# Kernel optimization log

Hardware: AMD Instinct MI355X
Metric: run time of the kernel (lower is better)

## Reference

```python
import jax, jax.numpy as jnp
import numpy as np

N_NODES = 50000


def gcn_conv(x, edge_index, W, b):
    # PyG GCNConv: add self-loops, symmetric normalization, then aggregate.
    n = x.shape[0]
    loop = jnp.arange(n, dtype=edge_index.dtype)
    src = jnp.concatenate([edge_index[0], loop])  # [E+N]
    dst = jnp.concatenate([edge_index[1], loop])  # [E+N]
    deg = jax.ops.segment_sum(jnp.ones_like(dst, dtype=x.dtype), dst, num_segments=n)
    dinv = jnp.where(deg > 0, jax.lax.rsqrt(deg), 0.0)
    norm = dinv[src] * dinv[dst]                  # [E+N]
    xw = x @ W                                     # [N, out]
    msg = xw[src] * norm[:, None]                  # [E+N, out]
    out = jax.ops.segment_sum(msg, dst, num_segments=n)
    return out + b


def setup_inputs() -> dict:
    key = jax.random.key(0)
    ks = jax.random.split(key, 8)
    n, e, d, h, c = N_NODES, 800000, 128, 128, 40
    x = jax.random.normal(ks[0], (n, d), dtype=jnp.float32)
    edge_index = jax.random.randint(ks[1], (2, e), 0, n, dtype=jnp.int64)
    s = 0.05
    W1 = jax.random.normal(ks[2], (d, h), dtype=jnp.float32) * s
    b1 = jnp.zeros((h,), dtype=jnp.float32)
    W2 = jax.random.normal(ks[3], (h, h), dtype=jnp.float32) * s
    b2 = jnp.zeros((h,), dtype=jnp.float32)
    W3 = jax.random.normal(ks[4], (h, c), dtype=jnp.float32) * s
    b3 = jnp.zeros((c,), dtype=jnp.float32)
    return {"x": x, "edge_index": edge_index, "W1": W1, "b1": b1,
            "W2": W2, "b2": b2, "W3": W3, "b3": b3}


def reference(x, edge_index, W1, b1, W2, b2, W3, b3):
    # Block 0: GCNConv -> relu -> (dropout: identity in eval) -> residual
    h = jax.nn.relu(gcn_conv(x, edge_index, W1, b1)) + x
    # Block 1: GCNConv -> relu -> (dropout: identity in eval) -> residual
    h = jax.nn.relu(gcn_conv(h, edge_index, W2, b2)) + h
    # Final conv + log_softmax over classes
    out = gcn_conv(h, edge_index, W3, b3)
    return jax.nn.log_softmax(out, axis=1)
```

## Files before the change

kernel.cpp:

```cpp
#include <hip/hip_runtime.h>
#include <math.h>


#define HD 128
#define NC 40

typedef __attribute__((ext_vector_type(8))) short bfrag;
typedef __attribute__((ext_vector_type(4))) float facc;

__device__ __forceinline__ float4 fma4(float s, float4 w, float4 a) {
  a.x = fmaf(s, w.x, a.x);
  a.y = fmaf(s, w.y, a.y);
  a.z = fmaf(s, w.z, a.z);
  a.w = fmaf(s, w.w, a.w);
  return a;
}

__device__ __forceinline__ unsigned short f2bf(float f) {
  unsigned int u = __float_as_uint(f);
  u += 0x7FFFu + ((u >> 16) & 1u);
  return (unsigned short)(u >> 16);
}
__device__ __forceinline__ unsigned int packbf2(float a, float b) {
  return (unsigned int)f2bf(a) | ((unsigned int)f2bf(b) << 16);
}
__device__ __forceinline__ float bf2f(unsigned short v) {
  return __uint_as_float((unsigned int)v << 16);
}
__device__ __forceinline__ float2 bf2f2(unsigned int v) {
  float2 r;
  r.x = __uint_as_float(v << 16);
  r.y = __uint_as_float(v & 0xFFFF0000u);
  return r;
}
__device__ __forceinline__ float db(unsigned int u, int i) {
  return (float)(signed char)((u >> (8 * i)) & 0xFFu);
}

#define NCOPY 8


__global__ void k_init(int* __restrict__ cnt8, int* __restrict__ gtotal, int n8) {
  int i = blockIdx.x * 256 + threadIdx.x;
  if (i < n8) cnt8[i] = 0;
  if (i == 0) *gtotal = 0;
}

__global__ __launch_bounds__(256) void k_count_rank(
    const int* __restrict__ dst, int* __restrict__ cnt8,
    int* __restrict__ rank, int E, int n) {
  int e = blockIdx.x * 256 + threadIdx.x;
  if (e < E) {
    int copy = blockIdx.x & (NCOPY - 1);
    rank[e] = atomicAdd(&cnt8[copy * n + dst[e]], 1);
  }
}

__global__ __launch_bounds__(256) void k_alloc(
    const int* __restrict__ cnt8, int* __restrict__ row_start,
    int* __restrict__ row_end, int2* __restrict__ cinfo,
    float* __restrict__ dinv, int* __restrict__ gtotal, int n) {
  __shared__ int sh[256];
  __shared__ int base_sh;
  const int tid = threadIdx.x;
  int i = blockIdx.x * 256 + tid;
  int c[NCOPY];
  int v = 0;
  if (i < n) {
#pragma unroll
    for (int j = 0; j < NCOPY; ++j) {
      c[j] = cnt8[j * n + i];
      v += c[j];
    }
  }
  sh[tid] = v;
  __syncthreads();
  for (int off = 1; off < 256; off <<= 1) {
    int t = (tid >= off) ? sh[tid - off] : 0;
    __syncthreads();
    sh[tid] += t;
    __syncthreads();
  }
  if (tid == 255) base_sh = atomicAdd(gtotal, sh[255]);
  __syncthreads();
  if (i < n) {
    int start = base_sh + sh[tid] - v;
    float dv = rsqrtf((float)(v + 1));
    row_start[i] = start;
    row_end[i] = start + v;
    dinv[i] = dv;
    int base = start;
#pragma unroll
    for (int j = 0; j < NCOPY; ++j) {
      cinfo[(size_t)j * n + i] = make_int2(base, __float_as_int(dv));
      base += c[j];
    }
  }
}

__global__ __launch_bounds__(256) void k_fill(
    const int* __restrict__ src, const int* __restrict__ dst,
    const int* __restrict__ rank, const int2* __restrict__ cinfo,
    const float* __restrict__ dinv, int2* __restrict__ csr2, int E, int n) {
  int t = blockIdx.x * 256 + threadIdx.x;
  int nt = gridDim.x * 256;
#pragma unroll
  for (int q = 0; q < 4; ++q) {
    int e = t + q * nt;
    if (e < E) {
      int d = dst[e];
      int s = src[e];
      int r = rank[e];
      int copy = (e >> 8) & (NCOPY - 1);
      int2 ni = cinfo[(size_t)copy * n + d];
      float norm = dinv[s] * __int_as_float(ni.y);
      csr2[ni.x + r] = make_int2(s, __float_as_int(norm));
    }
  }
}


__global__ __launch_bounds__(256) void k_wprep(
    const float* __restrict__ W1, const float* __restrict__ W2,
    unsigned short* __restrict__ W1t, unsigned short* __restrict__ W2t) {
  const float* W = blockIdx.x ? W2 : W1;
  unsigned short* Wt = blockIdx.x ? W2t : W1t;
  __shared__ unsigned short sh[HD * 136];
#pragma unroll
  for (int i = 0; i < 16; ++i) {
    int f4 = i * 256 + threadIdx.x;
    int r = f4 >> 5;
    int c = (f4 & 31) * 4;
    float4 v = *(const float4*)(W + r * HD + c);
    sh[(c + 0) * 136 + r] = f2bf(v.x);
    sh[(c + 1) * 136 + r] = f2bf(v.y);
    sh[(c + 2) * 136 + r] = f2bf(v.z);
    sh[(c + 3) * 136 + r] = f2bf(v.w);
  }
  __syncthreads();
#pragma unroll
  for (int i = 0; i < 8; ++i) {
    int g = i * 256 + threadIdx.x;
    int nrow = g >> 4, k16 = g & 15;
    uint4 v = *(const uint4*)(&sh[nrow * 136 + k16 * 8]);
    *(uint4*)(Wt + (size_t)g * 8) = v;
  }
}


template <bool A_IS_F32>
__global__ __launch_bounds__(256) void gemm_mfma_f128(
    const float* __restrict__ Af, const unsigned short* __restrict__ Ab,
    const unsigned short* __restrict__ Wt,
    signed char* __restrict__ xw8, float* __restrict__ xscale, int n) {
  __shared__ unsigned short shWt[HD * 136];
  {
#pragma unroll
    for (int i = 0; i < 8; ++i) {
      int g = i * 256 + threadIdx.x;
      int nrow = g >> 4, k16 = g & 15;
      uint4 v = *(const uint4*)(Wt + (size_t)g * 8);
      *(uint4*)(&shWt[nrow * 136 + k16 * 8]) = v;
    }
  }

  const int lane = threadIdx.x & 63;
  const int w = threadIdx.x >> 6;
  const int m = blockIdx.x * 64 + w * 16 + (lane & 15);
  const int mc = min(m, n - 1);
  const int kbase = (lane >> 4) * 8;

  bfrag af[4];
  if constexpr (A_IS_F32) {
    const float* ap = Af + (size_t)mc * HD + kbase;
#pragma unroll
    for (int kk = 0; kk < 4; ++kk) {
      float4 lo = *(const float4*)(ap + kk * 32);
      float4 hi = *(const float4*)(ap + kk * 32 + 4);
      bfrag a;
      a[0] = (short)f2bf(lo.x); a[1] = (short)f2bf(lo.y);
      a[2] = (short)f2bf(lo.z); a[3] = (short)f2bf(lo.w);
      a[4] = (short)f2bf(hi.x); a[5] = (short)f2bf(hi.y);
      a[6] = (short)f2bf(hi.z); a[7] = (short)f2bf(hi.w);
      af[kk] = a;
    }
  } else {
    const unsigned short* ap = Ab + (size_t)mc * HD + kbase;
#pragma unroll
    for (int kk = 0; kk < 4; ++kk) af[kk] = *(const bfrag*)(ap + kk * 32);
  }

  __syncthreads();

  facc acc[8];
#pragma unroll
  for (int c = 0; c < 8; ++c) {
    acc[c][0] = 0.f; acc[c][1] = 0.f; acc[c][2] = 0.f; acc[c][3] = 0.f;
  }

#pragma unroll
  for (int kk = 0; kk < 4; ++kk) {
#pragma unroll
    for (int c = 0; c < 8; ++c) {
      bfrag bf = *(const bfrag*)(&shWt[(c * 16 + (lane & 15)) * 136 + kk * 32 + kbase]);
      acc[c] = __builtin_amdgcn_mfma_f32_16x16x32_bf16(af[kk], bf, acc[c], 0, 0, 0);
    }
  }

  float rmax[4];
#pragma unroll
  for (int q = 0; q < 4; ++q) {
    float mx = 0.f;
#pragma unroll
    for (int c = 0; c < 8; ++c) mx = fmaxf(mx, fabsf(acc[c][q]));
    rmax[q] = mx;
  }
#pragma unroll
  for (int off = 1; off < 16; off <<= 1) {
#pragma unroll
    for (int q = 0; q < 4; ++q) rmax[q] = fmaxf(rmax[q], __shfl_xor(rmax[q], off, 64));
  }

  const int rbase = blockIdx.x * 64 + w * 16 + (lane >> 4) * 4;
  const int col = lane & 15;
#pragma unroll
  for (int q = 0; q < 4; ++q) {
    int r = rbase + q;
    if (r < n) {
      float inv = (rmax[q] > 0.f) ? (127.f / rmax[q]) : 0.f;
      if (col == q) xscale[r] = rmax[q] * (1.f / 127.f);
#pragma unroll
      for (int c = 0; c < 8; ++c) {
        int v = __float2int_rn(acc[c][q] * inv);
        xw8[(size_t)r * HD + c * 16 + col] = (signed char)v;
      }
    }
  }
}


__global__ __launch_bounds__(320) void gemm_k128_f40(
    const float* __restrict__ A, const float* __restrict__ W,
    unsigned short* __restrict__ out, int n) {
  __shared__ float shW[HD * NC];
  {
    const float4* Wv = (const float4*)W;
    float4* shWv = (float4*)shW;
    for (int t = threadIdx.x; t < HD * NC / 4; t += 320) shWv[t] = Wv[t];
  }
  __syncthreads();

  const int cg = threadIdx.x % 10;
  const int rg = threadIdx.x / 10;
  const int jg = cg * 4;
  const int row0 = blockIdx.x * 128 + rg * 4;
  const int nm1 = n - 1;
  const float* a[4];
#pragma unroll
  for (int r = 0; r < 4; ++r) a[r] = A + (size_t)min(row0 + r, nm1) * HD;

  float4 acc[4];
#pragma unroll
  for (int r = 0; r < 4; ++r) acc[r] = make_float4(0.f, 0.f, 0.f, 0.f);

  for (int k = 0; k < HD; k += 4) {
    const float* wb = shW + k * NC + jg;
    float4 w0 = *(const float4*)(wb);
    float4 w1 = *(const float4*)(wb + NC);
    float4 w2 = *(const float4*)(wb + 2 * NC);
    float4 w3 = *(const float4*)(wb + 3 * NC);
#pragma unroll
    for (int r = 0; r < 4; ++r) {
      float4 xv = *(const float4*)(a[r] + k);
      acc[r] = fma4(xv.w, w3, fma4(xv.z, w2, fma4(xv.y, w1, fma4(xv.x, w0, acc[r]))));
    }
  }
#pragma unroll
  for (int r = 0; r < 4; ++r) {
    if (row0 + r < n) {
      uint2 p;
      p.x = packbf2(acc[r].x, acc[r].y);
      p.y = packbf2(acc[r].z, acc[r].w);
      *(uint2*)(out + (size_t)(row0 + r) * NC + jg) = p;
    }
  }
}


__global__ __launch_bounds__(256) void agg_f128(
    const signed char* __restrict__ xw8, const float* __restrict__ xscale,
    const float* __restrict__ resid, const float* __restrict__ bias,
    const float* __restrict__ dinv,
    const int* __restrict__ row_start, const int* __restrict__ row_end,
    const int2* __restrict__ csr2, float* __restrict__ out,
    unsigned short* __restrict__ hb, int n) {
  const int node = (blockIdx.x * 256 + threadIdx.x) >> 4;
  if (node >= n) return;
  const int li = threadIdx.x & 15;
  const int f0 = li * 8;

  float di = dinv[node];
  float4 b01 = *(const float4*)(bias + f0);
  float4 b23 = *(const float4*)(bias + f0 + 4);
  uint2 su = *(const uint2*)(xw8 + (size_t)node * HD + f0);
  float ssc = xscale[node] * di * di;
  float a0 = fmaf(db(su.x, 0), ssc, b01.x);
  float a1 = fmaf(db(su.x, 1), ssc, b01.y);
  float a2 = fmaf(db(su.x, 2), ssc, b01.z);
  float a3 = fmaf(db(su.x, 3), ssc, b01.w);
  float a4 = fmaf(db(su.y, 0), ssc, b23.x);
  float a5 = fmaf(db(su.y, 1), ssc, b23.y);
  float a6 = fmaf(db(su.y, 2), ssc, b23.z);
  float a7 = fmaf(db(su.y, 3), ssc, b23.w);

  int k = row_start[node];
  const int end = row_end[node];
  for (; k + 4 <= end; k += 4) {
    int2 c0 = csr2[k], c1 = csr2[k + 1], c2 = csr2[k + 2], c3 = csr2[k + 3];
    uint2 u0 = *(const uint2*)(xw8 + (size_t)c0.x * HD + f0);
    uint2 u1 = *(const uint2*)(xw8 + (size_t)c1.x * HD + f0);
    uint2 u2 = *(const uint2*)(xw8 + (size_t)c2.x * HD + f0);
    uint2 u3 = *(const uint2*)(xw8 + (size_t)c3.x * HD + f0);
    float w0 = __int_as_float(c0.y) * xscale[c0.x];
    float w1 = __int_as_float(c1.y) * xscale[c1.x];
    float w2 = __int_as_float(c2.y) * xscale[c2.x];
    float w3 = __int_as_float(c3.y) * xscale[c3.x];
    a0 = fmaf(db(u0.x, 0), w0, a0); a1 = fmaf(db(u0.x, 1), w0, a1);
    a2 = fmaf(db(u0.x, 2), w0, a2); a3 = fmaf(db(u0.x, 3), w0, a3);
    a4 = fmaf(db(u0.y, 0), w0, a4); a5 = fmaf(db(u0.y, 1), w0, a5);
    a6 = fmaf(db(u0.y, 2), w0, a6); a7 = fmaf(db(u0.y, 3), w0, a7);
    a0 = fmaf(db(u1.x, 0), w1, a0); a1 = fmaf(db(u1.x, 1), w1, a1);
    a2 = fmaf(db(u1.x, 2), w1, a2); a3 = fmaf(db(u1.x, 3), w1, a3);
    a4 = fmaf(db(u1.y, 0), w1, a4); a5 = fmaf(db(u1.y, 1), w1, a5);
    a6 = fmaf(db(u1.y, 2), w1, a6); a7 = fmaf(db(u1.y, 3), w1, a7);
    a0 = fmaf(db(u2.x, 0), w2, a0); a1 = fmaf(db(u2.x, 1), w2, a1);
    a2 = fmaf(db(u2.x, 2), w2, a2); a3 = fmaf(db(u2.x, 3), w2, a3);
    a4 = fmaf(db(u2.y, 0), w2, a4); a5 = fmaf(db(u2.y, 1), w2, a5);
    a6 = fmaf(db(u2.y, 2), w2, a6); a7 = fmaf(db(u2.y, 3), w2, a7);
    a0 = fmaf(db(u3.x, 0), w3, a0); a1 = fmaf(db(u3.x, 1), w3, a1);
    a2 = fmaf(db(u3.x, 2), w3, a2); a3 = fmaf(db(u3.x, 3), w3, a3);
    a4 = fmaf(db(u3.y, 0), w3, a4); a5 = fmaf(db(u3.y, 1), w3, a5);
    a6 = fmaf(db(u3.y, 2), w3, a6); a7 = fmaf(db(u3.y, 3), w3, a7);
  }
  for (; k < end; ++k) {
    int2 c = csr2[k];
    uint2 u = *(const uint2*)(xw8 + (size_t)c.x * HD + f0);
    float w = __int_as_float(c.y) * xscale[c.x];
    a0 = fmaf(db(u.x, 0), w, a0); a1 = fmaf(db(u.x, 1), w, a1);
    a2 = fmaf(db(u.x, 2), w, a2); a3 = fmaf(db(u.x, 3), w, a3);
    a4 = fmaf(db(u.y, 0), w, a4); a5 = fmaf(db(u.y, 1), w, a5);
    a6 = fmaf(db(u.y, 2), w, a6); a7 = fmaf(db(u.y, 3), w, a7);
  }

  float4 r0 = *(const float4*)(resid + (size_t)node * HD + f0);
  float4 r1 = *(const float4*)(resid + (size_t)node * HD + f0 + 4);
  float4 o0, o1;
  o0.x = fmaxf(a0, 0.f) + r0.x; o0.y = fmaxf(a1, 0.f) + r0.y;
  o0.z = fmaxf(a2, 0.f) + r0.z; o0.w = fmaxf(a3, 0.f) + r0.w;
  o1.x = fmaxf(a4, 0.f) + r1.x; o1.y = fmaxf(a5, 0.f) + r1.y;
  o1.z = fmaxf(a6, 0.f) + r1.z; o1.w = fmaxf(a7, 0.f) + r1.w;
  *(float4*)(out + (size_t)node * HD + f0) = o0;
  *(float4*)(out + (size_t)node * HD + f0 + 4) = o1;
  if (hb) {
    uint4 hv;
    hv.x = packbf2(o0.x, o0.y);
    hv.y = packbf2(o0.z, o0.w);
    hv.z = packbf2(o1.x, o1.y);
    hv.w = packbf2(o1.z, o1.w);
    *(uint4*)(hb + (size_t)node * HD + f0) = hv;
  }
}


__global__ __launch_bounds__(256) void agg_f40_lsm(
    const unsigned short* __restrict__ xw, const float* __restrict__ dinv,
    const int* __restrict__ row_start, const int* __restrict__ row_end,
    const int2* __restrict__ csr2, const float* __restrict__ bias,
    float* __restrict__ out, int n) {
  const int node = (blockIdx.x * 256 + threadIdx.x) >> 4;
  if (node >= n) return;
  const int li = threadIdx.x & 15;
  const bool act = li < 10;
  const int f0 = li * 4;

  float a0 = 0.f, a1 = 0.f, a2 = 0.f, a3 = 0.f;
  float di = dinv[node];
  if (act) {
    float4 bv = *(const float4*)(bias + f0);
    uint2 su = *(const uint2*)(xw + (size_t)node * NC + f0);
    float2 s0 = bf2f2(su.x), s1 = bf2f2(su.y);
    float ssc = di * di;
    a0 = fmaf(s0.x, ssc, bv.x);
    a1 = fmaf(s0.y, ssc, bv.y);
    a2 = fmaf(s1.x, ssc, bv.z);
    a3 = fmaf(s1.y, ssc, bv.w);
  }

  int k = row_start[node];
  const int end = row_end[node];
  for (; k + 4 <= end; k += 4) {
    int2 c0 = csr2[k], c1 = csr2[k + 1], c2 = csr2[k + 2], c3 = csr2[k + 3];
    if (act) {
      uint2 u0 = *(const uint2*)(xw + (size_t)c0.x * NC + f0);
      uint2 u1 = *(const uint2*)(xw + (size_t)c1.x * NC + f0);
      uint2 u2 = *(const uint2*)(xw + (size_t)c2.x * NC + f0);
      uint2 u3 = *(const uint2*)(xw + (size_t)c3.x * NC + f0);
      float w0 = __int_as_float(c0.y), w1 = __int_as_float(c1.y);
      float w2 = __int_as_float(c2.y), w3 = __int_as_float(c3.y);
      float2 p, q;
      p = bf2f2(u0.x); q = bf2f2(u0.y);
      a0 = fmaf(p.x, w0, a0); a1 = fmaf(p.y, w0, a1);
      a2 = fmaf(q.x, w0, a2); a3 = fmaf(q.y, w0, a3);
      p = bf2f2(u1.x); q = bf2f2(u1.y);
      a0 = fmaf(p.x, w1, a0); a1 = fmaf(p.y, w1, a1);
      a2 = fmaf(q.x, w1, a2); a3 = fmaf(q.y, w1, a3);
      p = bf2f2(u2.x); q = bf2f2(u2.y);
      a0 = fmaf(p.x, w2, a0); a1 = fmaf(p.y, w2, a1);
      a2 = fmaf(q.x, w2, a2); a3 = fmaf(q.y, w2, a3);
      p = bf2f2(u3.x); q = bf2f2(u3.y);
      a0 = fmaf(p.x, w3, a0); a1 = fmaf(p.y, w3, a1);
      a2 = fmaf(q.x, w3, a2); a3 = fmaf(q.y, w3, a3);
    }
  }
  for (; k < end; ++k) {
    int2 c = csr2[k];
    if (act) {
      uint2 u = *(const uint2*)(xw + (size_t)c.x * NC + f0);
      float w = __int_as_float(c.y);
      float2 p = bf2f2(u.x), q = bf2f2(u.y);
      a0 = fmaf(p.x, w, a0); a1 = fmaf(p.y, w, a1);
      a2 = fmaf(q.x, w, a2); a3 = fmaf(q.y, w, a3);
    }
  }

  float m = act ? fmaxf(fmaxf(a0, a1), fmaxf(a2, a3)) : -3.0e38f;
  m = fmaxf(m, __shfl_xor(m, 1, 64));
  m = fmaxf(m, __shfl_xor(m, 2, 64));
  m = fmaxf(m, __shfl_xor(m, 4, 64));
  m = fmaxf(m, __shfl_xor(m, 8, 64));
  float s = act ? (expf(a0 - m) + expf(a1 - m) + expf(a2 - m) + expf(a3 - m)) : 0.f;
  s += __shfl_xor(s, 1, 64);
  s += __shfl_xor(s, 2, 64);
  s += __shfl_xor(s, 4, 64);
  s += __shfl_xor(s, 8, 64);
  if (act) {
    float lse = m + logf(s);
    float4 o;
    o.x = a0 - lse; o.y = a1 - lse; o.z = a2 - lse; o.w = a3 - lse;
    *(float4*)(out + (size_t)node * NC + f0) = o;
  }
}


extern "C" void kernel_launch(void* const* d_in, const int* in_sizes, int n_in,
                              void* d_out, int out_size, void* d_ws, size_t ws_size,
                              hipStream_t stream) {
  const float* x  = (const float*)d_in[0];
  const int*   ei = (const int*)d_in[1];
  const float* W1 = (const float*)d_in[2];
  const float* b1 = (const float*)d_in[3];
  const float* W2 = (const float*)d_in[4];
  const float* b2 = (const float*)d_in[5];
  const float* W3 = (const float*)d_in[6];
  const float* b3 = (const float*)d_in[7];
  float* out = (float*)d_out;

  const int n = in_sizes[0] / HD;
  const int E = in_sizes[1] / 2;
  const int* src = ei;
  const int* dst = ei + E;

  char* ws = (char*)d_ws;
  size_t off = 0;
  auto carve = [&](size_t bytes) -> void* {
    void* p = ws + off;
    off += (bytes + 255) & ~(size_t)255;
    return p;
  };
  int*   cnt8      = (int*)carve((size_t)n * NCOPY * 4);
  int*   row_start = (int*)carve((size_t)n * 4);
  int*   row_end   = (int*)carve((size_t)n * 4);
  float* dinv      = (float*)carve((size_t)n * 4);
  int2*  cinfo     = (int2*)carve((size_t)n * NCOPY * 8);
  int*   gtotal    = (int*)carve(256);
  unsigned short* w1t = (unsigned short*)carve((size_t)HD * HD * 2);
  unsigned short* w2t = (unsigned short*)carve((size_t)HD * HD * 2);
  int2*  csr2      = (int2*)carve((size_t)E * 8);
  signed char* xw8 = (signed char*)carve((size_t)n * HD);
  float* xscale    = (float*)carve((size_t)n * 4);
  unsigned short* xw40 = (unsigned short*)carve((size_t)n * NC * 2);
  unsigned short* hb  = (unsigned short*)carve((size_t)n * HD * 2);
  float* bufB      = (float*)carve((size_t)n * HD * 4);
  int*   rank      = (int*)bufB;

  const int gn8  = (n * NCOPY + 255) / 256;
  const int gE1  = (E + 255) / 256;
  const int gE4  = (E + 1023) / 1024;
  const int gA   = (n + 15) / 16;
  const int gM   = (n + 63) / 64;
  const int g40  = (n + 127) / 128;

  k_init<<<gn8, 256, 0, stream>>>(cnt8, gtotal, n * NCOPY);
  k_wprep<<<2, 256, 0, stream>>>(W1, W2, w1t, w2t);
  k_count_rank<<<gE1, 256, 0, stream>>>(dst, cnt8, rank, E, n);
  k_alloc<<<(n + 255) / 256, 256, 0, stream>>>(cnt8, row_start, row_end, cinfo, dinv, gtotal, n);
  k_fill<<<gE4, 256, 0, stream>>>(src, dst, rank, cinfo, dinv, csr2, E, n);

  gemm_mfma_f128<true><<<gM, 256, 0, stream>>>(x, (const unsigned short*)nullptr, w1t, xw8, xscale, n);
  agg_f128<<<gA, 256, 0, stream>>>(xw8, xscale, x, b1, dinv, row_start, row_end, csr2, bufB, hb, n);

  gemm_mfma_f128<false><<<gM, 256, 0, stream>>>((const float*)nullptr, hb, w2t, xw8, xscale, n);
  agg_f128<<<gA, 256, 0, stream>>>(xw8, xscale, bufB, b2, dinv, row_start, row_end, csr2, bufB,
                                   (unsigned short*)nullptr, n);

  gemm_k128_f40<<<g40, 320, 0, stream>>>(bufB, W3, xw40, n);
  agg_f40_lsm<<<gA, 256, 0, stream>>>(xw40, dinv, row_start, row_end, csr2, b3, out, n);
}
```

Measured before the change: 186.4 us.

## Use bf16 MFMA for final 40-class GEMM and skip fp32 layer-2 output

Result: faster. 168.2 us (-9.7%).

```diff
diff --git a/kernel.cpp b/kernel.cpp
--- a/kernel.cpp
+++ b/kernel.cpp
@@ -7,14 +7,6 @@
 
 typedef __attribute__((ext_vector_type(8))) short bfrag;
 typedef __attribute__((ext_vector_type(4))) float facc;
-
-__device__ __forceinline__ float4 fma4(float s, float4 w, float4 a) {
-  a.x = fmaf(s, w.x, a.x);
-  a.y = fmaf(s, w.y, a.y);
-  a.z = fmaf(s, w.z, a.z);
-  a.w = fmaf(s, w.w, a.w);
-  return a;
-}
 
 __device__ __forceinline__ unsigned short f2bf(float f) {
   unsigned int u = __float_as_uint(f);
@@ -23,9 +15,6 @@
 }
 __device__ __forceinline__ unsigned int packbf2(float a, float b) {
   return (unsigned int)f2bf(a) | ((unsigned int)f2bf(b) << 16);
-}
-__device__ __forceinline__ float bf2f(unsigned short v) {
-  return __uint_as_float((unsigned int)v << 16);
 }
 __device__ __forceinline__ float2 bf2f2(unsigned int v) {
   float2 r;
@@ -102,20 +91,15 @@
     const int* __restrict__ src, const int* __restrict__ dst,
     const int* __restrict__ rank, const int2* __restrict__ cinfo,
     const float* __restrict__ dinv, int2* __restrict__ csr2, int E, int n) {
-  int t = blockIdx.x * 256 + threadIdx.x;
-  int nt = gridDim.x * 256;
-#pragma unroll
-  for (int q = 0; q < 4; ++q) {
-    int e = t + q * nt;
-    if (e < E) {
-      int d = dst[e];
-      int s = src[e];
-      int r = rank[e];
-      int copy = (e >> 8) & (NCOPY - 1);
-      int2 ni = cinfo[(size_t)copy * n + d];
-      float norm = dinv[s] * __int_as_float(ni.y);
-      csr2[ni.x + r] = make_int2(s, __float_as_int(norm));
-    }
+  int e = blockIdx.x * 256 + threadIdx.x;
+  if (e < E) {
+    int d = dst[e];
+    int s = src[e];
+    int r = rank[e];
+    int copy = (e >> 8) & (NCOPY - 1);
+    int2 ni = cinfo[(size_t)copy * n + d];
+    float norm = dinv[s] * __int_as_float(ni.y);
+    csr2[ni.x + r] = make_int2(s, __float_as_int(norm));
   }
 }
 
@@ -147,6 +131,34 @@
   }
 }
 
+__global__ __launch_bounds__(256) void k_wprep3(
+    const float* __restrict__ W3, unsigned short* __restrict__ W3t) {
+  __shared__ unsigned short sh[48 * 136];
+  for (int i = threadIdx.x; i < 48 * 136; i += 256) sh[i] = 0;
+  __syncthreads();
+#pragma unroll
+  for (int i = 0; i < 5; ++i) {
+    int f4 = i * 256 + threadIdx.x;
+    if (f4 < 1280) {
+      int r = f4 / 10;
+      int c = (f4 % 10) * 4;
+      float4 v = *(const float4*)(W3 + r * NC + c);
+      sh[(c + 0) * 136 + r] = f2bf(v.x);
+      sh[(c + 1) * 136 + r] = f2bf(v.y);
+      sh[(c + 2) * 136 + r] = f2bf(v.z);
+      sh[(c + 3) * 136 + r] = f2bf(v.w);
+    }
+  }
+  __syncthreads();
+#pragma unroll
+  for (int i = 0; i < 3; ++i) {
+    int g = i * 256 + threadIdx.x;
+    int nrow = g >> 4, k16 = g & 15;
+    uint4 v = *(const uint4*)(&sh[nrow * 136 + k16 * 8]);
+    *(uint4*)(W3t + (size_t)g * 8) = v;
+  }
+}
+
 
 template <bool A_IS_F32>
 __global__ __launch_bounds__(256) void gemm_mfma_f128(
@@ -239,49 +251,59 @@
 }
 
 
-__global__ __launch_bounds__(320) void gemm_k128_f40(
-    const float* __restrict__ A, const float* __restrict__ W,
+__global__ __launch_bounds__(256) void gemm_mfma_f40(
+    const unsigned short* __restrict__ Ab,
+    const unsigned short* __restrict__ Wt,
     unsigned short* __restrict__ out, int n) {
-  __shared__ float shW[HD * NC];
+  __shared__ unsigned short shWt[48 * 136];
   {
-    const float4* Wv = (const float4*)W;
-    float4* shWv = (float4*)shW;
-    for (int t = threadIdx.x; t < HD * NC / 4; t += 320) shWv[t] = Wv[t];
-  }
-  __syncthreads();
-
-  const int cg = threadIdx.x % 10;
-  const int rg = threadIdx.x / 10;
-  const int jg = cg * 4;
-  const int row0 = blockIdx.x * 128 + rg * 4;
-  const int nm1 = n - 1;
-  const float* a[4];
-#pragma unroll
-  for (int r = 0; r < 4; ++r) a[r] = A + (size_t)min(row0 + r, nm1) * HD;
-
-  float4 acc[4];
-#pragma unroll
-  for (int r = 0; r < 4; ++r) acc[r] = make_float4(0.f, 0.f, 0.f, 0.f);
-
-  for (int k = 0; k < HD; k += 4) {
-    const float* wb = shW + k * NC + jg;
-    float4 w0 = *(const float4*)(wb);
-    float4 w1 = *(const float4*)(wb + NC);
-    float4 w2 = *(const float4*)(wb + 2 * NC);
-    float4 w3 = *(const float4*)(wb + 3 * NC);
-#pragma unroll
-    for (int r = 0; r < 4; ++r) {
-      float4 xv = *(const float4*)(a[r] + k);
-      acc[r] = fma4(xv.w, w3, fma4(xv.z, w2, fma4(xv.y, w1, fma4(xv.x, w0, acc[r]))));
-    }
-  }
-#pragma unroll
-  for (int r = 0; r < 4; ++r) {
-    if (row0 + r < n) {
-      uint2 p;
-      p.x = packbf2(acc[r].x, acc[r].y);
-      p.y = packbf2(acc[r].z, acc[r].w);
-      *(uint2*)(out + (size_t)(row0 + r) * NC + jg) = p;
+#pragma unroll
+    for (int i = 0; i < 3; ++i) {
+      int g = i * 256 + threadIdx.x;
+      int nrow = g >> 4, k16 = g & 15;
+      uint4 v = *(const uint4*)(Wt + (size_t)g * 8);
+      *(uint4*)(&shWt[nrow * 136 + k16 * 8]) = v;
+    }
+  }
+
+  const int lane = threadIdx.x & 63;
+  const int w = threadIdx.x >> 6;
+  const int m = blockIdx.x * 64 + w * 16 + (lane & 15);
+  const int mc = min(m, n - 1);
+  const int kbase = (lane >> 4) * 8;
+
+  bfrag af[4];
+  const unsigned short* ap = Ab + (size_t)mc * HD + kbase;
+#pragma unroll
+  for (int kk = 0; kk < 4; ++kk) af[kk] = *(const bfrag*)(ap + kk * 32);
+
+  __syncthreads();
+
+  facc acc[3];
+#pragma unroll
+  for (int c = 0; c < 3; ++c) {
+    acc[c][0] = 0.f; acc[c][1] = 0.f; acc[c][2] = 0.f; acc[c][3] = 0.f;
+  }
+#pragma unroll
+  for (int kk = 0; kk < 4; ++kk) {
+#pragma unroll
+    for (int c = 0; c < 3; ++c) {
+      bfrag bf = *(const bfrag*)(&shWt[(c * 16 + (lane & 15)) * 136 + kk * 32 + kbase]);
+      acc[c] = __builtin_amdgcn_mfma_f32_16x16x32_bf16(af[kk], bf, acc[c], 0, 0, 0);
+    }
+  }
+
+  const int rbase = blockIdx.x * 64 + w * 16 + (lane >> 4) * 4;
+  const int col = lane & 15;
+#pragma unroll
+  for (int c = 0; c < 3; ++c) {
+    int j = c * 16 + col;
+    if (j < NC) {
+#pragma unroll
+      for (int q = 0; q < 4; ++q) {
+        int r = rbase + q;
+        if (r < n) out[(size_t)r * NC + j] = f2bf(acc[c][q]);
+      }
     }
   }
 }
@@ -359,8 +381,10 @@
   o0.z = fmaxf(a2, 0.f) + r0.z; o0.w = fmaxf(a3, 0.f) + r0.w;
   o1.x = fmaxf(a4, 0.f) + r1.x; o1.y = fmaxf(a5, 0.f) + r1.y;
   o1.z = fmaxf(a6, 0.f) + r1.z; o1.w = fmaxf(a7, 0.f) + r1.w;
-  *(float4*)(out + (size_t)node * HD + f0) = o0;
-  *(float4*)(out + (size_t)node * HD + f0 + 4) = o1;
+  if (out) {
+    *(float4*)(out + (size_t)node * HD + f0) = o0;
+    *(float4*)(out + (size_t)node * HD + f0 + 4) = o1;
+  }
   if (hb) {
     uint4 hv;
     hv.x = packbf2(o0.x, o0.y);
@@ -485,6 +509,7 @@
   int*   gtotal    = (int*)carve(256);
   unsigned short* w1t = (unsigned short*)carve((size_t)HD * HD * 2);
   unsigned short* w2t = (unsigned short*)carve((size_t)HD * HD * 2);
+  unsigned short* w3t = (unsigned short*)carve((size_t)48 * HD * 2);
   int2*  csr2      = (int2*)carve((size_t)E * 8);
   signed char* xw8 = (signed char*)carve((size_t)n * HD);
   float* xscale    = (float*)carve((size_t)n * 4);
@@ -495,24 +520,23 @@
 
   const int gn8  = (n * NCOPY + 255) / 256;
   const int gE1  = (E + 255) / 256;
-  const int gE4  = (E + 1023) / 1024;
   const int gA   = (n + 15) / 16;
   const int gM   = (n + 63) / 64;
-  const int g40  = (n + 127) / 128;
 
   k_init<<<gn8, 256, 0, stream>>>(cnt8, gtotal, n * NCOPY);
   k_wprep<<<2, 256, 0, stream>>>(W1, W2, w1t, w2t);
+  k_wprep3<<<1, 256, 0, stream>>>(W3, w3t);
   k_count_rank<<<gE1, 256, 0, stream>>>(dst, cnt8, rank, E, n);
   k_alloc<<<(n + 255) / 256, 256, 0, stream>>>(cnt8, row_start, row_end, cinfo, dinv, gtotal, n);
-  k_fill<<<gE4, 256, 0, stream>>>(src, dst, rank, cinfo, dinv, csr2, E, n);
+  k_fill<<<gE1, 256, 0, stream>>>(src, dst, rank, cinfo, dinv, csr2, E, n);
 
   gemm_mfma_f128<true><<<gM, 256, 0, stream>>>(x, (const unsigned short*)nullptr, w1t, xw8, xscale, n);
   agg_f128<<<gA, 256, 0, stream>>>(xw8, xscale, x, b1, dinv, row_start, row_end, csr2, bufB, hb, n);
 
   gemm_mfma_f128<false><<<gM, 256, 0, stream>>>((const float*)nullptr, hb, w2t, xw8, xscale, n);
-  agg_f128<<<gA, 256, 0, stream>>>(xw8, xscale, bufB, b2, dinv, row_start, row_end, csr2, bufB,
-                                   (unsigned short*)nullptr, n);
-
-  gemm_k128_f40<<<g40, 320, 0, stream>>>(bufB, W3, xw40, n);
+  agg_f128<<<gA, 256, 0, stream>>>(xw8, xscale, bufB, b2, dinv, row_start, row_end, csr2,
+                                   (float*)nullptr, hb, n);
+
+  gemm_mfma_f40<<<gM, 256, 0, stream>>>(hb, w3t, xw40, n);
   agg_f40_lsm<<<gA, 256, 0, stream>>>(xw40, dinv, row_start, row_end, csr2, b3, out, n);
 }
```
